# Performance work log

Hardware: AMD Instinct MI355X
Metric: run time of the kernel (lower is better)

Reference implementation:

```python
import jax, jax.numpy as jnp
import numpy as np

DIM = 512
NUM_HEADS = 8


def setup_inputs() -> dict:
    key = jax.random.key(0)
    ks = jax.random.split(key, 9)
    B, C, H, W = 8, DIM, 32, 32
    s = 1.0 / np.sqrt(DIM)  # conv-style init scale
    return {
        "x": jax.random.normal(ks[0], (B, C, H, W), jnp.float32),
        "Wq": jax.random.normal(ks[1], (DIM, DIM), jnp.float32) * s,
        "bq": jnp.zeros((DIM,), jnp.float32),
        "Wk": jax.random.normal(ks[2], (DIM, DIM), jnp.float32) * s,
        "bk": jnp.zeros((DIM,), jnp.float32),
        "Wv": jax.random.normal(ks[3], (DIM, DIM), jnp.float32) * s,
        "bv": jnp.zeros((DIM,), jnp.float32),
        "Wo": jax.random.normal(ks[4], (DIM, DIM), jnp.float32) * s,
        "bo": jnp.zeros((DIM,), jnp.float32),
    }


def _proj(x, W, b):
    # 1x1 conv == per-pixel linear over channels: [out_c, in_c] x [b, in_c, h, w]
    return jnp.einsum('oc,bchw->bohw', W, x) + b[None, :, None, None]


def reference(x, Wq, bq, Wk, bk, Wv, bv, Wo, bo):
    b, c, h, w = x.shape
    g = NUM_HEADS
    dh = c // g  # per-head channels
    q = _proj(x, Wq, bq)
    k = _proj(x, Wk, bk)
    v = _proj(x, Wv, bv)
    # 'b (g c) h w -> (b g) c (h w)'
    def split_heads(t):
        return t.reshape(b, g, dh, h * w).reshape(b * g, dh, h * w)
    q, k, v = split_heads(q), split_heads(k), split_heads(v)
    # note: scale uses full dim (as in the source), not per-head dim
    a = jnp.einsum('bcs,bct->bst', q, k) / jnp.sqrt(jnp.float32(c))
    a = jax.nn.softmax(a, axis=-1)  # dropout is identity at inference
    o = jnp.einsum('bst,bct->bcs', a, v)  # [(b g), dh, s]
    o = o.reshape(b, g * dh, h, w)  # '(b g) c (h w) -> b (g c) h w'
    return x + _proj(o, Wo, bo)
```

## Files before the change

kernel.cpp:

```cpp
#include <hip/hip_runtime.h>

typedef unsigned short u16;
typedef __attribute__((ext_vector_type(8))) short short8;
typedef __attribute__((ext_vector_type(4))) short sh4;
typedef __attribute__((ext_vector_type(2))) int int2v;
typedef __attribute__((ext_vector_type(4))) float floatx4;

__device__ __forceinline__ float b2f(u16 u) {
  unsigned int x = ((unsigned int)u) << 16;
  return __builtin_bit_cast(float, x);
}
__device__ __forceinline__ u16 f2b(float f) {
  unsigned int x = __builtin_bit_cast(unsigned int, f);
  unsigned int r = (x + 0x7FFFu + ((x >> 16) & 1u)) >> 16;
  return (u16)r;
}
__device__ __forceinline__ unsigned int pk2bf(float a, float b) {
  unsigned int ua = __builtin_bit_cast(unsigned int, a) + 0x8000u;
  unsigned int ub = __builtin_bit_cast(unsigned int, b) + 0x8000u;
  return __builtin_amdgcn_perm(ub, ua, 0x07060302u);
}

#if __has_builtin(__builtin_amdgcn_mfma_f32_16x16x16bf16_1k)
#define MFMA16(a, b, c) __builtin_amdgcn_mfma_f32_16x16x16bf16_1k((a), (b), (c), 0, 0, 0)
#define MFMA16_DRAIN()
#else
__device__ __forceinline__ floatx4 mfma16_fb(sh4 a, sh4 b, floatx4 c) {
  asm volatile("s_nop 1\n\tv_mfma_f32_16x16x16_bf16 %0, %1, %2, %0"
               : "+v"(c) : "v"(a), "v"(b));
  return c;
}
#define MFMA16(a, b, c) mfma16_fb((a), (b), (c))
#define MFMA16_DRAIN() asm volatile("s_nop 7\n\ts_nop 7\n\ts_nop 7")
#endif

#if __has_builtin(__builtin_amdgcn_exp2f)
#define EXP2F(x) __builtin_amdgcn_exp2f(x)
#else
#define EXP2F(x) __expf((x) * 0.6931471805599453f)
#endif

#define MFMA32(a, b, c) __builtin_amdgcn_mfma_f32_16x16x32_bf16((a), (b), (c), 0, 0, 0)

#define GLL16(g, l) __builtin_amdgcn_global_load_lds(                         \
    (const __attribute__((address_space(1))) unsigned int*)(g),               \
    (__attribute__((address_space(3))) unsigned int*)(l), 16, 0, 0)

#define SC_LOG2E 0.06375872f

__device__ __forceinline__ int detect_fp32(const u16* __restrict__ x) {
  __shared__ int cnt;
  if (threadIdx.x == 0) cnt = 0;
  __syncthreads();
  int c = 0;
  if (threadIdx.x < 256) {
#pragma unroll
    for (int i = 0; i < 16; ++i) {
      u16 u = x[threadIdx.x * 16 + i];
      if (((u >> 7) & 0xFF) >= 0xC8) c++;
    }
  }
  if (c) atomicAdd(&cnt, c);
  __syncthreads();
  return cnt > 32;
}

__global__ __launch_bounds__(256) void prep(
    const u16* __restrict__ x,
    const u16* w0, const u16* w1, const u16* w2, const u16* w3,
    const u16* c0, const u16* c1, const u16* c2, const u16* c3,
    u16* __restrict__ xT, u16* __restrict__ Wc, u16* __restrict__ bc, int b0) {
  const int fp32 = detect_fp32(x);
  const int tid = threadIdx.x;
  if (blockIdx.y < 8) {
    __shared__ u16 t[64][65];
    const int lb = blockIdx.z, b = b0 + lb;
    const int p0 = blockIdx.x * 64, cc0 = blockIdx.y * 64;
    const int tx = tid & 63, ty = tid >> 6;
    if (fp32) {
      const float* xb = (const float*)x + (long)b * 524288;
#pragma unroll
      for (int i = 0; i < 16; ++i) {
        int c = ty + i * 4;
        t[c][tx] = f2b(xb[(long)(cc0 + c) * 1024 + p0 + tx]);
      }
    } else {
      const u16* xb = x + (long)b * 524288;
#pragma unroll
      for (int i = 0; i < 16; ++i) {
        int c = ty + i * 4;
        t[c][tx] = xb[(long)(cc0 + c) * 1024 + p0 + tx];
      }
    }
    __syncthreads();
    u16* xTb = xT + (long)lb * 524288;
#pragma unroll
    for (int i = 0; i < 16; ++i) {
      int p = ty + i * 4;
      xTb[(long)(p0 + p) * 512 + cc0 + tx] = t[tx][p];
    }
  } else {
    const u16* srcs[8] = {w0, w1, w2, w3, c0, c1, c2, c3};
    const int nthreads = gridDim.z * 16 * 256;
    const int flat = (blockIdx.z * 16 + blockIdx.x) * 256 + tid;
    for (int vi = flat; vi < 131072; vi += nthreads) {
      int w = vi >> 15;
      int off = (vi & 32767) * 8;
      u16* dst = Wc + w * 262144 + off;
      if (fp32) {
        const float* s = (const float*)srcs[w] + off;
        u16 tmp[8];
#pragma unroll
        for (int r = 0; r < 8; ++r) tmp[r] = f2b(s[r]);
        *(int4*)dst = *(const int4*)tmp;
      } else {
        *(int4*)dst = *(const int4*)(srcs[w] + off);
      }
    }
    for (int gi = flat; gi < 2048; gi += nthreads) {
      int t2 = gi >> 9;
      bc[gi] = fp32 ? f2b(((const float*)srcs[4 + t2])[gi & 511]) : srcs[4 + t2][gi & 511];
    }
  }
}

struct GemmLds64 {
  u16 As0[128][32], As1[128][32];
  u16 Bs0[128][32], Bs1[128][32];
};

__device__ __forceinline__ void gemm_core64(const u16* __restrict__ A, int lda,
                                            const u16* __restrict__ B, int ldb,
                                            int m0, int n0, int K,
                                            GemmLds64& lds, floatx4 (&acc)[4][4]) {
  const int tid = threadIdx.x;
  const int wave = tid >> 6, lane = tid & 63;
  const int quad = lane >> 4, l15 = lane & 15;
  const int wm = (wave >> 1) * 64, wn = (wave & 1) * 64;
  const int lrow = lane >> 2, lcol = (lane & 3) * 8;
  for (int k0 = 0; k0 < K; k0 += 64) {
    __syncthreads();
#pragma unroll
    for (int it = 0; it < 2; ++it) {
      const int rbase = wave * 32 + it * 16;
      const u16* Ar = A + (long)(m0 + rbase + lrow) * lda + k0 + lcol;
      GLL16(Ar, &lds.As0[rbase][0]);
      GLL16(Ar + 32, &lds.As1[rbase][0]);
      const u16* Br = B + (long)(n0 + rbase + lrow) * ldb + k0 + lcol;
      GLL16(Br, &lds.Bs0[rbase][0]);
      GLL16(Br + 32, &lds.Bs1[rbase][0]);
    }
    __syncthreads();
    short8 af[4], bf[4];
#pragma unroll
    for (int i = 0; i < 4; ++i)
      af[i] = *(const short8*)&lds.As0[wm + i * 16 + l15][quad * 8];
#pragma unroll
    for (int j = 0; j < 4; ++j)
      bf[j] = *(const short8*)&lds.Bs0[wn + j * 16 + l15][quad * 8];
#pragma unroll
    for (int i = 0; i < 4; ++i)
#pragma unroll
      for (int j = 0; j < 4; ++j)
        acc[i][j] = MFMA32(af[i], bf[j], acc[i][j]);
#pragma unroll
    for (int i = 0; i < 4; ++i)
      af[i] = *(const short8*)&lds.As1[wm + i * 16 + l15][quad * 8];
#pragma unroll
    for (int j = 0; j < 4; ++j)
      bf[j] = *(const short8*)&lds.Bs1[wn + j * 16 + l15][quad * 8];
#pragma unroll
    for (int i = 0; i < 4; ++i)
#pragma unroll
      for (int j = 0; j < 4; ++j)
        acc[i][j] = MFMA32(af[i], bf[j], acc[i][j]);
  }
}

__global__ __launch_bounds__(256) void gemm_qkv(
    const u16* __restrict__ xT, const u16* __restrict__ Wc,
    const u16* __restrict__ bc, u16* __restrict__ Qt, u16* __restrict__ Kt,
    u16* __restrict__ Vv) {
  __shared__ GemmLds64 lds;
  const long bz = blockIdx.y;
  const u16* xb = xT + bz * 524288;
  const int bx = blockIdx.x;
  const int qk = bx < 64;
  const int t = qk ? bx : bx - 64;
  const int m0 = (t >> 3) * 128, n0 = (t & 7) * 128;
  const u16* A = qk ? xb : (Wc + 524288);
  const u16* B = qk ? Wc : xb;
  floatx4 acc[4][4] = {};
  gemm_core64(A, 512, B, 512, m0, n0, 512, lds, acc);
  const int lane = threadIdx.x & 63, wave = threadIdx.x >> 6;
  const int quad = lane >> 4, l15 = lane & 15;
  const int wm = (wave >> 1) * 64, wn = (wave & 1) * 64;
  if (qk) {
    u16* Qz = Qt + bz * 524288;
    u16* Kz = Kt + bz * 524288;
#pragma unroll
    for (int i = 0; i < 4; ++i)
#pragma unroll
      for (int j = 0; j < 4; ++j)
#pragma unroll
        for (int r = 0; r < 4; ++r) {
          int gm = m0 + wm + i * 16 + quad * 4 + r;
          int gn = n0 + wn + j * 16 + l15;
          float v = acc[i][j][r] + b2f(bc[gn]);
          if (gn < 512) Qz[(long)gm * 512 + gn] = f2b(v * SC_LOG2E);
          else Kz[(long)gm * 512 + gn - 512] = f2b(v);
        }
  } else {
    u16* Vz = Vv + bz * 524288;
    const u16* bv = bc + 1024;
#pragma unroll
    for (int i = 0; i < 4; ++i)
#pragma unroll
      for (int j = 0; j < 4; ++j)
#pragma unroll
        for (int r = 0; r < 4; ++r) {
          int gm = m0 + wm + i * 16 + quad * 4 + r;
          int gn = n0 + wn + j * 16 + l15;
          float v = acc[i][j][r] + b2f(bv[gm]);
          Vz[(long)gm * 1024 + gn] = f2b(v);
        }
  }
}

struct OutLds64 {
  u16 As0[128][32], As1[128][32];
  u16 Bs0[64][32], Bs1[64][32];
};

__global__ __launch_bounds__(256) void gemm_out(
    const u16* __restrict__ Wo, const u16* __restrict__ bo,
    const u16* __restrict__ Ow, const u16* __restrict__ xraw,
    u16* __restrict__ out) {
  const int fp32 = detect_fp32(xraw);
  __shared__ OutLds64 lds;
  const long bz = blockIdx.z;
  const u16* B = Ow + bz * 524288;
  const int m0 = blockIdx.y * 128, n0 = blockIdx.x * 64;
  const int tid = threadIdx.x;
  const int wave = tid >> 6, lane = tid & 63;
  const int quad = lane >> 4, l15 = lane & 15;
  const int lrow = lane >> 2, lcol = (lane & 3) * 8;

  floatx4 acc[2][4] = {};

  for (int k0 = 0; k0 < 512; k0 += 64) {
    __syncthreads();
    {
      const int ra = wave * 32;
      const u16* A0 = Wo + (long)(m0 + ra + lrow) * 512 + k0 + lcol;
      const u16* A1 = Wo + (long)(m0 + ra + 16 + lrow) * 512 + k0 + lcol;
      GLL16(A0, &lds.As0[ra][0]);
      GLL16(A0 + 32, &lds.As1[ra][0]);
      GLL16(A1, &lds.As0[ra + 16][0]);
      GLL16(A1 + 32, &lds.As1[ra + 16][0]);
      const u16* Br = B + (long)(n0 + wave * 16 + lrow) * 512 + k0 + lcol;
      GLL16(Br, &lds.Bs0[wave * 16][0]);
      GLL16(Br + 32, &lds.Bs1[wave * 16][0]);
    }
    __syncthreads();
#pragma unroll
    for (int i = 0; i < 2; ++i) {
      short8 af = *(const short8*)&lds.As0[wave * 32 + i * 16 + l15][quad * 8];
#pragma unroll
      for (int j = 0; j < 4; ++j) {
        short8 bf = *(const short8*)&lds.Bs0[j * 16 + l15][quad * 8];
        acc[i][j] = MFMA32(af, bf, acc[i][j]);
      }
    }
#pragma unroll
    for (int i = 0; i < 2; ++i) {
      short8 af = *(const short8*)&lds.As1[wave * 32 + i * 16 + l15][quad * 8];
#pragma unroll
      for (int j = 0; j < 4; ++j) {
        short8 bf = *(const short8*)&lds.Bs1[j * 16 + l15][quad * 8];
        acc[i][j] = MFMA32(af, bf, acc[i][j]);
      }
    }
  }

#pragma unroll
  for (int i = 0; i < 2; ++i)
#pragma unroll
    for (int j = 0; j < 4; ++j)
#pragma unroll
      for (int r = 0; r < 4; ++r) {
        int gm = m0 + wave * 32 + i * 16 + quad * 4 + r;
        int gn = n0 + j * 16 + l15;
        float v = acc[i][j][r] + b2f(bo[gm]);
        long idx = bz * 524288 + (long)gm * 1024 + gn;
        if (fp32) {
          v += ((const float*)xraw)[idx];
          ((float*)out)[idx] = v;
        } else {
          v += b2f(xraw[idx]);
          out[idx] = f2b(v);
        }
      }
}

#define AP 72
__global__ __launch_bounds__(512, 4) void attn(
    const u16* __restrict__ Qt, const u16* __restrict__ Kt,
    const u16* __restrict__ V, u16* __restrict__ O) {
  __shared__ alignas(16) u16 Ks[2][64][AP];
  __shared__ alignas(16) u16 Vs[2][64][AP];
  const int bg = blockIdx.x;
  const int lb = bg >> 3, head = bg & 7;
  const int s0 = blockIdx.y * 128;
  const int tid = threadIdx.x;
  const int wave = tid >> 6, lane = tid & 63;
  const int quad = lane >> 4, l15 = lane & 15;

  const u16* Qb = Qt + (long)lb * 524288 + head * 64;
  const u16* Kb = Kt + (long)lb * 524288 + head * 64;
  const u16* Vb = V + (long)(lb * 512 + head * 64) * 1024;
  u16* Ob = O + (long)lb * 524288 + head * 64;

  short8 bq[2];
#pragma unroll
  for (int kk = 0; kk < 2; ++kk)
    bq[kk] = *(const short8*)&Qb[(long)(s0 + wave * 16 + l15) * 512 +
                                 kk * 32 + quad * 8];

  const int r0 = tid >> 3, o0 = (tid & 7) * 8;
  int4 kreg, vreg;
  kreg = *(const int4*)&Kb[(long)r0 * 512 + o0];
  vreg = *(const int4*)&Vb[(long)r0 * 1024 + o0];
  *(int4*)&Ks[0][r0][o0] = kreg;
  *(int4*)&Vs[0][r0][o0] = vreg;

  floatx4 acc[4] = {};
  floatx4 accl = {};
  const sh4 ones = {(short)0x3F80, (short)0x3F80, (short)0x3F80, (short)0x3F80};

  for (int it16 = 0; it16 < 16; ++it16) {
    const int buf = it16 & 1;
    const int t0n = (it16 + 1) * 64;
    if (it16 < 15) {
      kreg = *(const int4*)&Kb[(long)(t0n + r0) * 512 + o0];
      vreg = *(const int4*)&Vb[(long)r0 * 1024 + t0n + o0];
    }
    __syncthreads();

    floatx4 p[4] = {};
#pragma unroll
    for (int kk = 0; kk < 2; ++kk) {
      short8 ak[4];
#pragma unroll
      for (int mi = 0; mi < 4; ++mi)
        ak[mi] = *(const short8*)&Ks[buf][mi * 16 + l15][kk * 32 + quad * 8];
#pragma unroll
      for (int mi = 0; mi < 4; ++mi)
        p[mi] = MFMA32(ak[mi], bq[kk], p[mi]);
    }

    sh4 pk[4];
#pragma unroll
    for (int mi = 0; mi < 4; ++mi) {
      float e0 = EXP2F(p[mi][0]);
      float e1 = EXP2F(p[mi][1]);
      float e2 = EXP2F(p[mi][2]);
      float e3 = EXP2F(p[mi][3]);
      int2v w;
      w.x = (int)pk2bf(e0, e1);
      w.y = (int)pk2bf(e2, e3);
      pk[mi] = __builtin_bit_cast(sh4, w);
    }

#pragma unroll
    for (int mi = 0; mi < 4; ++mi) accl = MFMA16(ones, pk[mi], accl);

#pragma unroll
    for (int mi = 0; mi < 4; ++mi) {
      sh4 av[4];
#pragma unroll
      for (int ci = 0; ci < 4; ++ci)
        av[ci] = *(const sh4*)&Vs[buf][ci * 16 + l15][mi * 16 + quad * 4];
#pragma unroll
      for (int ci = 0; ci < 4; ++ci)
        acc[ci] = MFMA16(av[ci], pk[mi], acc[ci]);
    }

    if (it16 < 15) {
      const int nb = 1 - buf;
      *(int4*)&Ks[nb][r0][o0] = kreg;
      *(int4*)&Vs[nb][r0][o0] = vreg;
    }
  }
  MFMA16_DRAIN();

  const float inv = 1.0f / accl[0];

  u16 (*Os)[AP] = (u16(*)[AP]) & Ks[0][0][0];
  __syncthreads();
#pragma unroll
  for (int ci = 0; ci < 4; ++ci) {
    int2v w;
    w.x = (int)pk2bf(acc[ci][0] * inv, acc[ci][1] * inv);
    w.y = (int)pk2bf(acc[ci][2] * inv, acc[ci][3] * inv);
    *(int2v*)&Os[wave * 16 + l15][ci * 16 + quad * 4] = w;
  }
  __syncthreads();
  {
    const int srow = tid >> 2, c16 = (tid & 3) * 16;
    *(int4*)&Ob[(long)(s0 + srow) * 512 + c16] = *(const int4*)&Os[srow][c16];
    *(int4*)&Ob[(long)(s0 + srow) * 512 + c16 + 8] = *(const int4*)&Os[srow][c16 + 8];
  }
}

extern "C" void kernel_launch(void* const* d_in, const int* in_sizes, int n_in,
                              void* d_out, int out_size, void* d_ws, size_t ws_size,
                              hipStream_t stream) {
  const u16* x  = (const u16*)d_in[0];
  const u16* Wq = (const u16*)d_in[1];
  const u16* bq = (const u16*)d_in[2];
  const u16* Wk = (const u16*)d_in[3];
  const u16* bk = (const u16*)d_in[4];
  const u16* Wv = (const u16*)d_in[5];
  const u16* bv = (const u16*)d_in[6];
  const u16* Wo = (const u16*)d_in[7];
  const u16* bo = (const u16*)d_in[8];
  u16* out = (u16*)d_out;
  u16* ws = (u16*)d_ws;

  const size_t PLAN_A_BYTES = 27267072;

  if (ws_size >= PLAN_A_BYTES) {
    u16* xT = ws;
    u16* Kt = ws + 4194304;
    u16* Vv = ws + 8388608;
    u16* Wc = ws + 12582912;
    u16* bc = ws + 13631488;
    u16* Qt = out;
    u16* Ow = xT;

    prep<<<dim3(16, 9, 8), 256, 0, stream>>>(x, Wq, Wk, Wv, Wo,
                                             bq, bk, bv, bo, xT, Wc, bc, 0);
    gemm_qkv<<<dim3(96, 8), 256, 0, stream>>>(xT, Wc, bc, Qt, Kt, Vv);
    attn<<<dim3(64, 8), 512, 0, stream>>>(Qt, Kt, Vv, Ow);
    gemm_out<<<dim3(16, 4, 8), 256, 0, stream>>>(Wc + 786432, bc + 1536, Ow, x, out);
  } else {
    u16* Ow = ws;
    u16* Kt = ws + 4194304;
    u16* Vv = ws + 6291456;
    u16* Wc = ws + 8388608;
    u16* bc = ws + 9437184;
    u16* Qt = out;

    for (int phase = 0; phase < 2; ++phase) {
      const int b0 = phase * 4;
      u16* xT = Ow + (long)phase * 2097152;
      prep<<<dim3(16, 9, 4), 256, 0, stream>>>(x, Wq, Wk, Wv, Wo,
                                               bq, bk, bv, bo, xT, Wc, bc, b0);
      gemm_qkv<<<dim3(96, 4), 256, 0, stream>>>(xT, Wc, bc, Qt, Kt, Vv);
      attn<<<dim3(32, 8), 512, 0, stream>>>(Qt, Kt, Vv, Ow + (long)b0 * 524288);
    }
    gemm_out<<<dim3(16, 4, 8), 256, 0, stream>>>(Wc + 786432, bc + 1536, Ow, x, out);
  }
}
```

Baseline: 163.5 us.

## Fuse attention and output projection into one persistent kernel with flag sync

Merges the attention kernel and the output-projection GEMM into a single launch. Each block first computes an attention tile, then publishes a per-(batch, row-chunk) completion flag and runs one output-GEMM tile, spinning until the attention rows it needs are ready. A second counter makes every block finish reading Q before any block overwrites the output buffer that also holds Q. This removes a kernel launch and lets the GEMM overlap with attention tail work, at the cost of a memset, spin-waits, and relying on all 512 blocks being co-resident to avoid deadlock.

```diff
diff --git a/kernel.cpp b/kernel.cpp
--- a/kernel.cpp
+++ b/kernel.cpp
@@ -47,6 +47,7 @@
     (__attribute__((address_space(3))) unsigned int*)(l), 16, 0, 0)
 
 #define SC_LOG2E 0.06375872f
+#define AP 72
 
 __device__ __forceinline__ int detect_fp32(const u16* __restrict__ x) {
   __shared__ int cnt;
@@ -227,6 +228,292 @@
   }
 }
 
+union AOLds {
+  struct { u16 Ks[2][64][AP]; u16 Vs[2][64][AP]; } at;
+  struct { u16 As0[128][32], As1[128][32], Bs0[64][32], Bs1[64][32]; } gm;
+};
+
+__global__ __launch_bounds__(512, 4) void attn_out(
+    const u16* __restrict__ Qt, const u16* __restrict__ Kt,
+    const u16* __restrict__ V, u16* __restrict__ Ow,
+    const u16* __restrict__ Wo, const u16* __restrict__ bo,
+    const u16* __restrict__ xraw, u16* __restrict__ outp,
+    unsigned* __restrict__ flags, unsigned* __restrict__ qrdy) {
+  __shared__ AOLds sm;
+  const int bid = blockIdx.x, tid = threadIdx.x;
+  const int fp32 = detect_fp32(xraw);
+  const int wave = tid >> 6, lane = tid & 63;
+  const int quad = lane >> 4, l15 = lane & 15;
+
+  {
+    const int bg = bid & 63, lb = bg >> 3, head = bg & 7;
+    const int s0 = (bid >> 6) * 128;
+    const u16* Qb = Qt + (long)lb * 524288 + head * 64;
+    const u16* Kb = Kt + (long)lb * 524288 + head * 64;
+    const u16* Vb = V + (long)(lb * 512 + head * 64) * 1024;
+    u16* Ob = Ow + (long)lb * 524288 + head * 64;
+
+    short8 bq[2];
+#pragma unroll
+    for (int kk = 0; kk < 2; ++kk)
+      bq[kk] = *(const short8*)&Qb[(long)(s0 + wave * 16 + l15) * 512 +
+                                   kk * 32 + quad * 8];
+
+    const int r0 = tid >> 3, o0 = (tid & 7) * 8;
+    int4 kreg = *(const int4*)&Kb[(long)r0 * 512 + o0];
+    int4 vreg = *(const int4*)&Vb[(long)r0 * 1024 + o0];
+    *(int4*)&sm.at.Ks[0][r0][o0] = kreg;
+    *(int4*)&sm.at.Vs[0][r0][o0] = vreg;
+
+    __syncthreads();
+    if (tid == 0)
+      __hip_atomic_fetch_add(qrdy, 1u, __ATOMIC_RELEASE, __HIP_MEMORY_SCOPE_AGENT);
+
+    floatx4 acc[4] = {};
+    floatx4 accl = {};
+    const sh4 ones = {(short)0x3F80, (short)0x3F80, (short)0x3F80, (short)0x3F80};
+
+    for (int it16 = 0; it16 < 16; ++it16) {
+      const int buf = it16 & 1;
+      const int t0n = (it16 + 1) * 64;
+      if (it16 < 15) {
+        kreg = *(const int4*)&Kb[(long)(t0n + r0) * 512 + o0];
+        vreg = *(const int4*)&Vb[(long)r0 * 1024 + t0n + o0];
+      }
+      __syncthreads();
+
+      floatx4 p[4] = {};
+#pragma unroll
+      for (int kk = 0; kk < 2; ++kk) {
+        short8 ak[4];
+#pragma unroll
+        for (int mi = 0; mi < 4; ++mi)
+          ak[mi] = *(const short8*)&sm.at.Ks[buf][mi * 16 + l15][kk * 32 + quad * 8];
+#pragma unroll
+        for (int mi = 0; mi < 4; ++mi)
+          p[mi] = MFMA32(ak[mi], bq[kk], p[mi]);
+      }
+
+      sh4 pk[4];
+#pragma unroll
+      for (int mi = 0; mi < 4; ++mi) {
+        float e0 = EXP2F(p[mi][0]);
+        float e1 = EXP2F(p[mi][1]);
+        float e2 = EXP2F(p[mi][2]);
+        float e3 = EXP2F(p[mi][3]);
+        int2v w;
+        w.x = (int)pk2bf(e0, e1);
+        w.y = (int)pk2bf(e2, e3);
+        pk[mi] = __builtin_bit_cast(sh4, w);
+      }
+
+#pragma unroll
+      for (int mi = 0; mi < 4; ++mi) accl = MFMA16(ones, pk[mi], accl);
+
+#pragma unroll
+      for (int mi = 0; mi < 4; ++mi) {
+        sh4 av[4];
+#pragma unroll
+        for (int ci = 0; ci < 4; ++ci)
+          av[ci] = *(const sh4*)&sm.at.Vs[buf][ci * 16 + l15][mi * 16 + quad * 4];
+#pragma unroll
+        for (int ci = 0; ci < 4; ++ci)
+          acc[ci] = MFMA16(av[ci], pk[mi], acc[ci]);
+      }
+
+      if (it16 < 15) {
+        const int nb = 1 - buf;
+        *(int4*)&sm.at.Ks[nb][r0][o0] = kreg;
+        *(int4*)&sm.at.Vs[nb][r0][o0] = vreg;
+      }
+    }
+    MFMA16_DRAIN();
+
+    const float inv = 1.0f / accl[0];
+    u16 (*Os)[AP] = (u16(*)[AP]) & sm.at.Ks[0][0][0];
+    __syncthreads();
+#pragma unroll
+    for (int ci = 0; ci < 4; ++ci) {
+      int2v w;
+      w.x = (int)pk2bf(acc[ci][0] * inv, acc[ci][1] * inv);
+      w.y = (int)pk2bf(acc[ci][2] * inv, acc[ci][3] * inv);
+      *(int2v*)&Os[wave * 16 + l15][ci * 16 + quad * 4] = w;
+    }
+    __syncthreads();
+    {
+      const int srow = tid >> 2, c16 = (tid & 3) * 16;
+      *(int4*)&Ob[(long)(s0 + srow) * 512 + c16] = *(const int4*)&Os[srow][c16];
+      *(int4*)&Ob[(long)(s0 + srow) * 512 + c16 + 8] = *(const int4*)&Os[srow][c16 + 8];
+    }
+    __syncthreads();
+    if (tid == 0) {
+      __threadfence();
+      __hip_atomic_fetch_add(&flags[lb * 8 + (bid >> 6)], 1u,
+                             __ATOMIC_RELEASE, __HIP_MEMORY_SCOPE_AGENT);
+    }
+  }
+
+  {
+    const int b = bid >> 6, t = bid & 63;
+    const int m0 = (t >> 4) * 128, n0 = (t & 15) * 64;
+    if (tid == 0) {
+      while (__hip_atomic_load(&flags[b * 8 + (n0 >> 7)], __ATOMIC_ACQUIRE,
+                               __HIP_MEMORY_SCOPE_AGENT) < 8u)
+        __builtin_amdgcn_s_sleep(8);
+    }
+    __syncthreads();
+    __threadfence();
+
+    const u16* B = Ow + (long)b * 524288;
+    const int lrow = lane >> 2, lcol = (lane & 3) * 8;
+    floatx4 acc[4] = {};
+
+    for (int k0 = 0; k0 < 512; k0 += 64) {
+      __syncthreads();
+      {
+        const u16* Ar = Wo + (long)(m0 + wave * 16 + lrow) * 512 + k0 + lcol;
+        GLL16(Ar, &sm.gm.As0[wave * 16][0]);
+        GLL16(Ar + 32, &sm.gm.As1[wave * 16][0]);
+        const int wv = wave & 3;
+        const u16* Br = B + (long)(n0 + wv * 16 + lrow) * 512 + k0 +
+                        ((wave >> 2) ? 32 : 0) + lcol;
+        if (wave < 4) GLL16(Br, &sm.gm.Bs0[wv * 16][0]);
+        else GLL16(Br, &sm.gm.Bs1[wv * 16][0]);
+      }
+      __syncthreads();
+      short8 af = *(const short8*)&sm.gm.As0[wave * 16 + l15][quad * 8];
+#pragma unroll
+      for (int j = 0; j < 4; ++j) {
+        short8 bf = *(const short8*)&sm.gm.Bs0[j * 16 + l15][quad * 8];
+        acc[j] = MFMA32(af, bf, acc[j]);
+      }
+      af = *(const short8*)&sm.gm.As1[wave * 16 + l15][quad * 8];
+#pragma unroll
+      for (int j = 0; j < 4; ++j) {
+        short8 bf = *(const short8*)&sm.gm.Bs1[j * 16 + l15][quad * 8];
+        acc[j] = MFMA32(af, bf, acc[j]);
+      }
+    }
+
+    if (tid == 0) {
+      while (__hip_atomic_load(qrdy, __ATOMIC_ACQUIRE,
+                               __HIP_MEMORY_SCOPE_AGENT) < 512u)
+        __builtin_amdgcn_s_sleep(2);
+    }
+    __syncthreads();
+
+#pragma unroll
+    for (int j = 0; j < 4; ++j)
+#pragma unroll
+      for (int r = 0; r < 4; ++r) {
+        int gm = m0 + wave * 16 + quad * 4 + r;
+        int gn = n0 + j * 16 + l15;
+        float v = acc[j][r] + b2f(bo[gm]);
+        long idx = (long)b * 524288 + (long)gm * 1024 + gn;
+        if (fp32) {
+          v += ((const float*)xraw)[idx];
+          ((float*)outp)[idx] = v;
+        } else {
+          v += b2f(xraw[idx]);
+          outp[idx] = f2b(v);
+        }
+      }
+  }
+}
+
+__global__ __launch_bounds__(512, 4) void attn(
+    const u16* __restrict__ Qt, const u16* __restrict__ Kt,
+    const u16* __restrict__ V, u16* __restrict__ O) {
+  __shared__ alignas(16) u16 Ks[2][64][AP];
+  __shared__ alignas(16) u16 Vs[2][64][AP];
+  const int bg = blockIdx.x;
+  const int lb = bg >> 3, head = bg & 7;
+  const int s0 = blockIdx.y * 128;
+  const int tid = threadIdx.x;
+  const int wave = tid >> 6, lane = tid & 63;
+  const int quad = lane >> 4, l15 = lane & 15;
+  const u16* Qb = Qt + (long)lb * 524288 + head * 64;
+  const u16* Kb = Kt + (long)lb * 524288 + head * 64;
+  const u16* Vb = V + (long)(lb * 512 + head * 64) * 1024;
+  u16* Ob = O + (long)lb * 524288 + head * 64;
+  short8 bq[2];
+#pragma unroll
+  for (int kk = 0; kk < 2; ++kk)
+    bq[kk] = *(const short8*)&Qb[(long)(s0 + wave * 16 + l15) * 512 + kk * 32 + quad * 8];
+  const int r0 = tid >> 3, o0 = (tid & 7) * 8;
+  int4 kreg = *(const int4*)&Kb[(long)r0 * 512 + o0];
+  int4 vreg = *(const int4*)&Vb[(long)r0 * 1024 + o0];
+  *(int4*)&Ks[0][r0][o0] = kreg;
+  *(int4*)&Vs[0][r0][o0] = vreg;
+  floatx4 acc[4] = {};
+  floatx4 accl = {};
+  const sh4 ones = {(short)0x3F80, (short)0x3F80, (short)0x3F80, (short)0x3F80};
+  for (int it16 = 0; it16 < 16; ++it16) {
+    const int buf = it16 & 1;
+    const int t0n = (it16 + 1) * 64;
+    if (it16 < 15) {
+      kreg = *(const int4*)&Kb[(long)(t0n + r0) * 512 + o0];
+      vreg = *(const int4*)&Vb[(long)r0 * 1024 + t0n + o0];
+    }
+    __syncthreads();
+    floatx4 p[4] = {};
+#pragma unroll
+    for (int kk = 0; kk < 2; ++kk) {
+      short8 ak[4];
+#pragma unroll
+      for (int mi = 0; mi < 4; ++mi)
+        ak[mi] = *(const short8*)&Ks[buf][mi * 16 + l15][kk * 32 + quad * 8];
+#pragma unroll
+      for (int mi = 0; mi < 4; ++mi) p[mi] = MFMA32(ak[mi], bq[kk], p[mi]);
+    }
+    sh4 pk[4];
+#pragma unroll
+    for (int mi = 0; mi < 4; ++mi) {
+      float e0 = EXP2F(p[mi][0]);
+      float e1 = EXP2F(p[mi][1]);
+      float e2 = EXP2F(p[mi][2]);
+      float e3 = EXP2F(p[mi][3]);
+      int2v w;
+      w.x = (int)pk2bf(e0, e1);
+      w.y = (int)pk2bf(e2, e3);
+      pk[mi] = __builtin_bit_cast(sh4, w);
+    }
+#pragma unroll
+    for (int mi = 0; mi < 4; ++mi) accl = MFMA16(ones, pk[mi], accl);
+#pragma unroll
+    for (int mi = 0; mi < 4; ++mi) {
+      sh4 av[4];
+#pragma unroll
+      for (int ci = 0; ci < 4; ++ci)
+        av[ci] = *(const sh4*)&Vs[buf][ci * 16 + l15][mi * 16 + quad * 4];
+#pragma unroll
+      for (int ci = 0; ci < 4; ++ci) acc[ci] = MFMA16(av[ci], pk[mi], acc[ci]);
+    }
+    if (it16 < 15) {
+      const int nb = 1 - buf;
+      *(int4*)&Ks[nb][r0][o0] = kreg;
+      *(int4*)&Vs[nb][r0][o0] = vreg;
+    }
+  }
+  MFMA16_DRAIN();
+  const float inv = 1.0f / accl[0];
+  u16 (*Os)[AP] = (u16(*)[AP]) & Ks[0][0][0];
+  __syncthreads();
+#pragma unroll
+  for (int ci = 0; ci < 4; ++ci) {
+    int2v w;
+    w.x = (int)pk2bf(acc[ci][0] * inv, acc[ci][1] * inv);
+    w.y = (int)pk2bf(acc[ci][2] * inv, acc[ci][3] * inv);
+    *(int2v*)&Os[wave * 16 + l15][ci * 16 + quad * 4] = w;
+  }
+  __syncthreads();
+  {
+    const int srow = tid >> 2, c16 = (tid & 3) * 16;
+    *(int4*)&Ob[(long)(s0 + srow) * 512 + c16] = *(const int4*)&Os[srow][c16];
+    *(int4*)&Ob[(long)(s0 + srow) * 512 + c16 + 8] = *(const int4*)&Os[srow][c16 + 8];
+  }
+}
+
 struct OutLds64 {
   u16 As0[128][32], As1[128][32];
   u16 Bs0[64][32], Bs1[64][32];
@@ -245,9 +532,7 @@
   const int wave = tid >> 6, lane = tid & 63;
   const int quad = lane >> 4, l15 = lane & 15;
   const int lrow = lane >> 2, lcol = (lane & 3) * 8;
-
   floatx4 acc[2][4] = {};
-
   for (int k0 = 0; k0 < 512; k0 += 64) {
     __syncthreads();
     {
@@ -282,7 +567,6 @@
       }
     }
   }
-
 #pragma unroll
   for (int i = 0; i < 2; ++i)
 #pragma unroll
@@ -301,116 +585,6 @@
           out[idx] = f2b(v);
         }
       }
-}
-
-#define AP 72
-__global__ __launch_bounds__(512, 4) void attn(
-    const u16* __restrict__ Qt, const u16* __restrict__ Kt,
-    const u16* __restrict__ V, u16* __restrict__ O) {
-  __shared__ alignas(16) u16 Ks[2][64][AP];
-  __shared__ alignas(16) u16 Vs[2][64][AP];
-  const int bg = blockIdx.x;
-  const int lb = bg >> 3, head = bg & 7;
-  const int s0 = blockIdx.y * 128;
-  const int tid = threadIdx.x;
-  const int wave = tid >> 6, lane = tid & 63;
-  const int quad = lane >> 4, l15 = lane & 15;
-
-  const u16* Qb = Qt + (long)lb * 524288 + head * 64;
-  const u16* Kb = Kt + (long)lb * 524288 + head * 64;
-  const u16* Vb = V + (long)(lb * 512 + head * 64) * 1024;
-  u16* Ob = O + (long)lb * 524288 + head * 64;
-
-  short8 bq[2];
-#pragma unroll
-  for (int kk = 0; kk < 2; ++kk)
-    bq[kk] = *(const short8*)&Qb[(long)(s0 + wave * 16 + l15) * 512 +
-                                 kk * 32 + quad * 8];
-
-  const int r0 = tid >> 3, o0 = (tid & 7) * 8;
-  int4 kreg, vreg;
-  kreg = *(const int4*)&Kb[(long)r0 * 512 + o0];
-  vreg = *(const int4*)&Vb[(long)r0 * 1024 + o0];
-  *(int4*)&Ks[0][r0][o0] = kreg;
-  *(int4*)&Vs[0][r0][o0] = vreg;
-
-  floatx4 acc[4] = {};
-  floatx4 accl = {};
-  const sh4 ones = {(short)0x3F80, (short)0x3F80, (short)0x3F80, (short)0x3F80};
-
-  for (int it16 = 0; it16 < 16; ++it16) {
-    const int buf = it16 & 1;
-    const int t0n = (it16 + 1) * 64;
-    if (it16 < 15) {
-      kreg = *(const int4*)&Kb[(long)(t0n + r0) * 512 + o0];
-      vreg = *(const int4*)&Vb[(long)r0 * 1024 + t0n + o0];
-    }
-    __syncthreads();
-
-    floatx4 p[4] = {};
-#pragma unroll
-    for (int kk = 0; kk < 2; ++kk) {
-      short8 ak[4];
-#pragma unroll
-      for (int mi = 0; mi < 4; ++mi)
-        ak[mi] = *(const short8*)&Ks[buf][mi * 16 + l15][kk * 32 + quad * 8];
-#pragma unroll
-      for (int mi = 0; mi < 4; ++mi)
-        p[mi] = MFMA32(ak[mi], bq[kk], p[mi]);
-    }
-
-    sh4 pk[4];
-#pragma unroll
-    for (int mi = 0; mi < 4; ++mi) {
-      float e0 = EXP2F(p[mi][0]);
-      float e1 = EXP2F(p[mi][1]);
-      float e2 = EXP2F(p[mi][2]);
-      float e3 = EXP2F(p[mi][3]);
-      int2v w;
-      w.x = (int)pk2bf(e0, e1);
-      w.y = (int)pk2bf(e2, e3);
-      pk[mi] = __builtin_bit_cast(sh4, w);
-    }
-
-#pragma unroll
-    for (int mi = 0; mi < 4; ++mi) accl = MFMA16(ones, pk[mi], accl);
-
-#pragma unroll
-    for (int mi = 0; mi < 4; ++mi) {
-      sh4 av[4];
-#pragma unroll
-      for (int ci = 0; ci < 4; ++ci)
-        av[ci] = *(const sh4*)&Vs[buf][ci * 16 + l15][mi * 16 + quad * 4];
-#pragma unroll
-      for (int ci = 0; ci < 4; ++ci)
-        acc[ci] = MFMA16(av[ci], pk[mi], acc[ci]);
-    }
-
-    if (it16 < 15) {
-      const int nb = 1 - buf;
-      *(int4*)&Ks[nb][r0][o0] = kreg;
-      *(int4*)&Vs[nb][r0][o0] = vreg;
-    }
-  }
-  MFMA16_DRAIN();
-
-  const float inv = 1.0f / accl[0];
-
-  u16 (*Os)[AP] = (u16(*)[AP]) & Ks[0][0][0];
-  __syncthreads();
-#pragma unroll
-  for (int ci = 0; ci < 4; ++ci) {
-    int2v w;
-    w.x = (int)pk2bf(acc[ci][0] * inv, acc[ci][1] * inv);
-    w.y = (int)pk2bf(acc[ci][2] * inv, acc[ci][3] * inv);
-    *(int2v*)&Os[wave * 16 + l15][ci * 16 + quad * 4] = w;
-  }
-  __syncthreads();
-  {
-    const int srow = tid >> 2, c16 = (tid & 3) * 16;
-    *(int4*)&Ob[(long)(s0 + srow) * 512 + c16] = *(const int4*)&Os[srow][c16];
-    *(int4*)&Ob[(long)(s0 + srow) * 512 + c16 + 8] = *(const int4*)&Os[srow][c16 + 8];
-  }
 }
 
 extern "C" void kernel_launch(void* const* d_in, const int* in_sizes, int n_in,
@@ -428,7 +602,7 @@
   u16* out = (u16*)d_out;
   u16* ws = (u16*)d_ws;
 
-  const size_t PLAN_A_BYTES = 27267072;
+  const size_t PLAN_A_BYTES = 27268096;
 
   if (ws_size >= PLAN_A_BYTES) {
     u16* xT = ws;
@@ -436,14 +610,17 @@
     u16* Vv = ws + 8388608;
     u16* Wc = ws + 12582912;
     u16* bc = ws + 13631488;
+    unsigned* flags = (unsigned*)(ws + 13633536);
+    unsigned* qrdy = flags + 64;
     u16* Qt = out;
     u16* Ow = xT;
 
+    hipMemsetAsync(flags, 0, 512, stream);
     prep<<<dim3(16, 9, 8), 256, 0, stream>>>(x, Wq, Wk, Wv, Wo,
                                              bq, bk, bv, bo, xT, Wc, bc, 0);
     gemm_qkv<<<dim3(96, 8), 256, 0, stream>>>(xT, Wc, bc, Qt, Kt, Vv);
-    attn<<<dim3(64, 8), 512, 0, stream>>>(Qt, Kt, Vv, Ow);
-    gemm_out<<<dim3(16, 4, 8), 256, 0, stream>>>(Wc + 786432, bc + 1536, Ow, x, out);
+    attn_out<<<512, 512, 0, stream>>>(Qt, Kt, Vv, Ow, Wc + 786432, bc + 1536,
+                                      x, out, flags, qrdy);
   } else {
     u16* Ow = ws;
     u16* Kt = ws + 4194304;
```

Result: slower. 329.1 us (+101.3%).
